# Performance work log

Hardware: AMD Instinct MI355X
Metric: run time of the kernel (lower is better)

The kernel has to match this reference:

```python
import jax, jax.numpy as jnp
import numpy as np

# ---- Clifford algebra Cl(4,1) setup -------------------------------------
SIG = [1, 1, 1, 1, -1]
GA = 1 << len(SIG)  # 32
B, S, E, H = 2, 512, 256, 8
HD = E // H


def _cayley_sign(sig):
    """sign[a,b] such that e_a * e_b = sign[a,b] * e_(a XOR b)."""
    n = len(sig)
    G = 1 << n
    M = np.zeros((G, G), np.float32)
    for a in range(G):
        for b in range(G):
            # canonical reordering sign
            ss = 0
            aa = a >> 1
            while aa:
                ss += bin(aa & b).count('1')
                aa >>= 1
            s = -1.0 if (ss & 1) else 1.0
            # metric contraction on shared basis vectors
            common = a & b
            for i in range(n):
                if (common >> i) & 1:
                    s *= sig[i]
            M[a, b] = s
    return M

SIGN = _cayley_sign(SIG)          # [GA, GA]
SIG_DIAG = np.diag(SIGN).copy()   # blade square signs (metric diagonal)


def _manifold_norm(x):
    # normalize each multivector over its GA components
    return x / jnp.sqrt(jnp.sum(x * x, axis=-1, keepdims=True) + 1e-6)


def _geo_linear(x, w):
    """Clifford linear layer: out[...,o,l] = sum_{i,m,n: m^n=l} w[o,i,m] x[...,i,n] sign(m,n).
    x: [B,S,In,GA], w: [Out,In,GA]. Loop over 32 fixed blades (signed permutation + GEMM)."""
    G = x.shape[-1]
    out = 0.0
    for m in range(G):
        perm = np.arange(G) ^ m              # n = m ^ l
        coeff = jnp.asarray(SIGN[m, perm])   # sign(m, n)
        xs = x[..., perm] * coeff            # [B,S,In,GA]
        out = out + jnp.einsum('oi,bsil->bsol', w[:, :, m], xs)
    return out


def _versor_linear(x, w):
    return _manifold_norm(_geo_linear(x, w))


def _forward(x, mask, wq, wk, wv, wo, gamma):
    b, s = x.shape[0], x.shape[1]
    q = _versor_linear(x, wq).reshape(b, s, H, HD, GA).transpose(0, 2, 1, 3, 4)
    k = _versor_linear(x, wk).reshape(b, s, H, HD, GA).transpose(0, 2, 1, 3, 4)
    v = _versor_linear(x, wv).reshape(b, s, H, HD, GA).transpose(0, 2, 1, 3, 4)
    q_flat = q.reshape(b * H, s, HD, GA)
    k_flat = k.reshape(b * H, s, HD, GA)
    sig_diag = jnp.asarray(SIG_DIAG)
    q_sig = q_flat * sig_diag                      # metric-weighted query
    scalar_score = jnp.einsum('bidl,bjdl->bij', q_sig, k_flat)   # [BH,S,S]
    q_norm_sq = jnp.sum(q_flat ** 2, axis=(-1, -2))[:, :, None]  # [BH,S,1]
    k_norm_sq = jnp.sum(k_flat ** 2, axis=(-1, -2))[:, None, :]  # [BH,1,S]
    bivector_norm = jnp.sqrt(jax.nn.relu(q_norm_sq * k_norm_sq - scalar_score ** 2) + 1e-6)
    score = (scalar_score + gamma * bivector_norm) / np.float32(np.sqrt(HD))
    # triangle update (seq > 1)
    score = score + 0.1 * jnp.matmul(jax.nn.softmax(score, axis=-1), score)
    score = score.reshape(b, H, s, s)
    score = jnp.where(mask[:, None, None, :] == 0, jnp.float32(-1e9), score)
    attn_probs = jax.nn.softmax(score, axis=-1)
    out = jnp.einsum('bhij,bhjdl->bhidl', attn_probs, v)
    out = out.transpose(0, 2, 1, 3, 4).reshape(b, s, E, GA)
    return _versor_linear(out, wo)


def setup_inputs() -> dict:
    key = jax.random.key(0)
    ks = jax.random.split(key, 6)
    std = np.float32((2.0 / (E * GA)) ** 0.5)
    x = jax.random.normal(ks[0], (B, S, E, GA), dtype=jnp.float32)
    wq = jax.random.normal(ks[1], (E, E, GA), dtype=jnp.float32) * std
    wk = jax.random.normal(ks[2], (E, E, GA), dtype=jnp.float32) * std
    wv = jax.random.normal(ks[3], (E, E, GA), dtype=jnp.float32) * std
    wo = jax.random.normal(ks[4], (E, E, GA), dtype=jnp.float32) * std
    gamma = jnp.asarray(0.1, dtype=jnp.float32)
    mask = jnp.ones((B, S), dtype=jnp.int32)
    return {'x': x, 'wq': wq, 'wk': wk, 'wv': wv, 'wo': wo, 'gamma': gamma, 'mask': mask}


def reference(x, wq, wk, wv, wo, gamma, mask):
    return _forward(x, mask, wq, wk, wv, wo, gamma)
```

## Files before the change

kernel.cpp:

```cpp
#include <hip/hip_runtime.h>
#include <stdint.h>

typedef unsigned short u16;
typedef unsigned int u32;
typedef __attribute__((ext_vector_type(8))) __bf16 bf16x8;
typedef __attribute__((ext_vector_type(4))) float f32x4;

#define DEVINL __device__ __forceinline__

DEVINL float bf2f(u16 u){ union{u32 i; float f;} c; c.i = ((u32)u)<<16; return c.f; }
DEVINL u16 f2bf(float f){ union{float f; u32 i;} c; c.f=f; u32 u=c.i; return (u16)((u + 0x7fffu + ((u>>16)&1u))>>16); }
DEVINL u32 pack2(float a, float b){ return (u32)f2bf(a) | ((u32)f2bf(b)<<16); }

DEVINL int sign_neg(int a, int b){
  int s = __popc((a>>1)&b) + __popc((a>>2)&b) + __popc((a>>3)&b) + __popc((a>>4)&b) + ((a&b)>>4);
  return s & 1;
}

struct GTab { int col[32][4]; int ph[32][4]; };
constexpr GTab make_gtab(){
  GTab g{};
  int gc[5][4] = {}; int gp[5][4] = {};
  for (int r=0;r<4;r++){
    const int a=(r>>1)&1, b=r&1;
    gc[0][r]=r^2; gp[0][r]=0;
    gc[1][r]=r^2; gp[1][r]= a?1:3;
    gc[2][r]=r^1; gp[2][r]= a?2:0;
    gc[3][r]=r^1; gp[3][r]=((a?2:0)+(b?1:3))&3;
    gc[4][r]=r;   gp[4][r]=(3+(a?2:0)+(b?2:0))&3;
  }
  for (int I=0;I<32;I++){
    for (int r=0;r<4;r++){ g.col[I][r]=r; g.ph[I][r]=0; }
    for (int bit=0;bit<5;bit++) if ((I>>bit)&1){
      for (int r=0;r<4;r++){
        const int c = g.col[I][r];
        g.ph[I][r]  = (g.ph[I][r] + gp[bit][c]) & 3;
        g.col[I][r] = gc[bit][c];
      }
    }
  }
  return g;
}
constexpr GTab GT = make_gtab();

DEVINL void mv2mat(const float (&x)[32], float (&Mre)[4][4], float (&Mim)[4][4]){
  #pragma unroll
  for (int r=0;r<4;r++)
    #pragma unroll
    for (int c=0;c<4;c++){ Mre[r][c]=0.f; Mim[r][c]=0.f; }
  #pragma unroll
  for (int l=0;l<32;l++){
    #pragma unroll
    for (int r=0;r<4;r++){
      constexpr const GTab& G = GT;
      const int c = G.col[l][r], p = G.ph[l][r];
      if (p==0) Mre[r][c] += x[l];
      else if (p==1) Mim[r][c] += x[l];
      else if (p==2) Mre[r][c] -= x[l];
      else Mim[r][c] -= x[l];
    }
  }
}

DEVINL void mat2mv(const float (&v)[4][8], float (&x)[32]){
  #pragma unroll
  for (int l=0;l<32;l++){
    float s = 0.f;
    #pragma unroll
    for (int r=0;r<4;r++){
      constexpr const GTab& G = GT;
      const int c = G.col[l][r], p = G.ph[l][r];
      if (p==0) s += v[c][r];
      else if (p==1) s += v[c][4+r];
      else if (p==2) s -= v[c][r];
      else s -= v[c][4+r];
    }
    x[l] = 0.25f*s;
  }
}

DEVINL void gload_lds16(const void* g, void* l){
  __builtin_amdgcn_global_load_lds(
    (const __attribute__((address_space(1))) void*)g,
    (__attribute__((address_space(3))) void*)l, 16, 0, 0);
}

__global__ __launch_bounds__(256) void k_v2m(const float* __restrict__ x, u16* __restrict__ Am){
  const int bs = blockIdx.x, i = threadIdx.x;
  const float* xp = x + ((size_t)bs*256 + i)*32;
  float xv[32];
  #pragma unroll
  for (int q=0;q<8;q++){
    float4 v = *(const float4*)(xp + q*4);
    xv[q*4+0]=v.x; xv[q*4+1]=v.y; xv[q*4+2]=v.z; xv[q*4+3]=v.w;
  }
  float Mre[4][4], Mim[4][4];
  mv2mat(xv, Mre, Mim);
  #pragma unroll
  for (int c=0;c<4;c++){
    u32 w0 = pack2(Mre[0][c], Mre[1][c]);
    u32 w1 = pack2(Mre[2][c], Mre[3][c]);
    u32 w2 = pack2(Mim[0][c], Mim[1][c]);
    u32 w3 = pack2(Mim[2][c], Mim[3][c]);
    *(uint4*)(Am + ((size_t)(bs*4+c))*2048 + i*8) = make_uint4(w0,w1,w2,w3);
  }
}

__global__ __launch_bounds__(256) void k_w2m(const float* __restrict__ wq, const float* __restrict__ wk,
                                             const float* __restrict__ wv, const float* __restrict__ wo,
                                             u16* __restrict__ Bfo){
  const int bid = blockIdx.x, i = threadIdx.x;
  const int wsel = bid>>8, o = bid&255;
  const float* w = wsel==0?wq: wsel==1?wk: wsel==2?wv: wo;
  const float* wp = w + ((size_t)o*256 + i)*32;
  float wv32[32];
  #pragma unroll
  for (int q=0;q<8;q++){
    float4 v = *(const float4*)(wp + q*4);
    wv32[q*4+0]=v.x; wv32[q*4+1]=v.y; wv32[q*4+2]=v.z; wv32[q*4+3]=v.w;
  }
  float Wre[4][4], Wim[4][4];
  mv2mat(wv32, Wre, Wim);
  u16* base = Bfo + (size_t)wsel*4194304 + (size_t)(i>>3)*131072 + (o>>1)*1024
            + ((i>>2)&1)*512;
  const int lanebase = (o&1)*8 + (i&3)*16;
  #pragma unroll
  for (int r8=0;r8<8;r8++){
    float e0,e1,e2,e3,e4,e5,e6,e7;
    if (r8<4){
      e0=Wre[r8][0]; e1=Wre[r8][1]; e2=Wre[r8][2]; e3=Wre[r8][3];
      e4=-Wim[r8][0]; e5=-Wim[r8][1]; e6=-Wim[r8][2]; e7=-Wim[r8][3];
    } else {
      e0=Wim[r8-4][0]; e1=Wim[r8-4][1]; e2=Wim[r8-4][2]; e3=Wim[r8-4][3];
      e4=Wre[r8-4][0]; e5=Wre[r8-4][1]; e6=Wre[r8-4][2]; e7=Wre[r8-4][3];
    }
    *(uint4*)(base + (lanebase + r8)*8) =
      make_uint4(pack2(e0,e1), pack2(e2,e3), pack2(e4,e5), pack2(e6,e7));
  }
}

template<int EPI>
__global__ __launch_bounds__(256) void k_mgemm(const u16* __restrict__ Am, const u16* __restrict__ Bfo,
                                               u16* __restrict__ qkv, float* __restrict__ dout,
                                               float* __restrict__ Nqp, float* __restrict__ Nkp){
  constexpr int NT = (EPI==0)?48:16;
  constexpr int NWG = 32*NT;
  __shared__ __align__(16) u16 SM[128*136];
  const int wg = blockIdx.x;
  const int bid = (wg&7)*(NWG/8) + (wg>>3);
  const int tn = bid>>5, tm = bid&31;
  const int row0 = tm*128, col0 = tn*128;
  const int sel   = (EPI==0)? (col0>>11) : 3;
  const int ncol0 = (EPI==0)? (col0&2047) : col0;
  const u16* Wsel = Bfo + (size_t)sel*4194304;
  const int t = threadIdx.x, lane = t&63, wid = t>>6;
  const int wm = wid>>1, wn = wid&1, lo = lane&15, hi = lane>>4;

  int boff[4][2];
  #pragma unroll
  for (int fn=0; fn<4; ++fn){
    const int nblk = (ncol0>>4) + wn*4 + fn;
    #pragma unroll
    for (int kk=0; kk<2; ++kk)
      boff[fn][kk] = (nblk*2+kk)*512 + lane*8;
  }

  f32x4 acc[4][4];
  #pragma unroll
  for(int a=0;a<4;a++){
    #pragma unroll
    for(int b=0;b<4;b++){ acc[a][b] = (f32x4){0.f,0.f,0.f,0.f}; }
  }

  const int sbase = (wid*4)*64;
  #pragma unroll
  for (int cc=0;cc<4;cc++){
    const int base = sbase + cc*64;
    const int idx = base + lane;
    const int rr = idx>>3, g = idx&7;
    gload_lds16(Am + (size_t)(row0+rr)*2048 + ((g^(rr&7))*8), SM + base*8);
  }

  int cbuf = 0;
  for (int kq=0; kq<32; ++kq){
    const u16* Wq = Wsel + (size_t)kq*131072;
    uint4 Br[8];
    #pragma unroll
    for (int fn=0; fn<4; ++fn){
      Br[fn*2+0] = *(const uint4*)(Wq + boff[fn][0]);
      Br[fn*2+1] = *(const uint4*)(Wq + boff[fn][1]);
    }
    if (kq == 0) asm volatile("s_waitcnt vmcnt(8)" ::: "memory");
    else         asm volatile("s_waitcnt vmcnt(4)" ::: "memory");
    __builtin_amdgcn_sched_barrier(0);
    __builtin_amdgcn_s_barrier();
    __builtin_amdgcn_sched_barrier(0);
    if (kq+1 < 32){
      #pragma unroll
      for (int cc=0;cc<4;cc++){
        const int base = sbase + cc*64;
        const int idx = base + lane;
        const int rr = idx>>3, g = idx&7;
        gload_lds16(Am + (size_t)(row0+rr)*2048 + (kq+1)*64 + ((g^(rr&7))*8),
                    SM + (cbuf^1)*8192 + base*8);
      }
    }
    const u16* Ab = SM + cbuf*8192;
    #pragma unroll
    for (int kk=0; kk<2; ++kk){
      bf16x8 af[4];
      #pragma unroll
      for (int f=0;f<4;f++){
        const int ra = wm*64 + f*16 + lo;
        const int jc = kk*4 + hi;
        af[f] = *(const bf16x8*)(Ab + ra*64 + ((jc^(ra&7))*8));
      }
      __builtin_amdgcn_s_setprio(1);
      #pragma unroll
      for (int fm=0;fm<4;fm++){
        #pragma unroll
        for (int fn=0;fn<4;fn++)
          acc[fm][fn] = __builtin_amdgcn_mfma_f32_16x16x32_bf16(
              af[fm], *(const bf16x8*)&Br[fn*2+kk], acc[fm][fn], 0,0,0);
      }
      __builtin_amdgcn_s_setprio(0);
    }
    cbuf ^= 1;
  }

  __syncthreads();
  #pragma unroll
  for (int fm=0;fm<4;fm++){
    #pragma unroll
    for (int r=0;r<4;r++){
      const int mL = wm*64 + fm*16 + hi*4 + r;
      #pragma unroll
      for (int fn=0;fn<4;fn++){
        const int nL = wn*64 + fn*16 + lo;
        SM[mL*136 + nL] = f2bf(acc[fm][fn][r]);
      }
    }
  }
  __syncthreads();
  const int bsL = t>>3, oLp = t&7;
  const int bs = (row0>>2) + bsL;
  const int o0w = ncol0>>3;
  float nsum = 0.f;
  #pragma unroll
  for (int u=0;u<2;u++){
    const int oL = oLp + u*8;
    float v[4][8];
    #pragma unroll
    for (int c=0;c<4;c++){
      uint4 q4 = *(const uint4*)(SM + (bsL*4+c)*136 + oL*8);
      v[c][0]=bf2f((u16)(q4.x&0xffffu)); v[c][1]=bf2f((u16)(q4.x>>16));
      v[c][2]=bf2f((u16)(q4.y&0xffffu)); v[c][3]=bf2f((u16)(q4.y>>16));
      v[c][4]=bf2f((u16)(q4.z&0xffffu)); v[c][5]=bf2f((u16)(q4.z>>16));
      v[c][6]=bf2f((u16)(q4.w&0xffffu)); v[c][7]=bf2f((u16)(q4.w>>16));
    }
    float xs[32];
    mat2mv(v, xs);
    float s = 0.f;
    #pragma unroll
    for (int l=0;l<32;l++) s += xs[l]*xs[l];
    const float rs = rsqrtf(s + 1e-6f);
    if constexpr (EPI==0){
      nsum += s/(s+1e-6f);
      if (sel == 0){
        #pragma unroll
        for (int l=0;l<32;l++) xs[l] = sign_neg(l,l)? -xs[l]*rs : xs[l]*rs;
      } else {
        #pragma unroll
        for (int l=0;l<32;l++) xs[l] *= rs;
      }
      u16* dst = qkv + ((size_t)bs*768 + sel*256 + o0w + oL)*32;
      #pragma unroll
      for (int q=0;q<4;q++)
        *(uint4*)(dst + q*8) = make_uint4(pack2(xs[q*8+0],xs[q*8+1]), pack2(xs[q*8+2],xs[q*8+3]),
                                          pack2(xs[q*8+4],xs[q*8+5]), pack2(xs[q*8+6],xs[q*8+7]));
    } else {
      float* dst = dout + ((size_t)bs*256 + o0w + oL)*32;
      #pragma unroll
      for (int q=0;q<8;q++)
        *(float4*)(dst + q*4) = make_float4(xs[q*4+0]*rs, xs[q*4+1]*rs, xs[q*4+2]*rs, xs[q*4+3]*rs);
    }
  }
  if constexpr (EPI==0){
    if (sel < 2){
      nsum += __shfl_xor(nsum,1); nsum += __shfl_xor(nsum,2); nsum += __shfl_xor(nsum,4);
      if ((t&7)==0){
        const int half = (o0w>>4)&1, h = o0w>>5;
        const int b = bs>>9, s_ = bs&511;
        float* nd = (sel==0)? Nqp : Nkp;
        nd[half*8192 + (b*8+h)*512 + s_] = nsum;
      }
    }
  }
}

DEVINL void mm_steps(const u16* Abase, int Astride, const u16* Bbase, int Bstride, int ksteps,
                     u16* Al, u16* Bl, f32x4 (&acc)[4][4], int lane, int wid){
  const int wm = wid>>1, wn = wid&1, lo = lane&15, hi = lane>>4;
  for (int s=0; s<ksteps; ++s){
    const int k0 = s*64;
    #pragma unroll
    for (int c=0;c<4;c++){
      const int gb = (wid*4+c)*64;
      const int idx = gb + lane;
      const int r = idx>>3, j = idx&7;
      const int sw = ((j^(r&7))*8);
      gload_lds16(Abase + (size_t)r*Astride + k0 + sw, Al + gb*8);
      gload_lds16(Bbase + (size_t)r*Bstride + k0 + sw, Bl + gb*8);
    }
    __syncthreads();
    #pragma unroll
    for (int kk=0; kk<2; ++kk){
      bf16x8 af[4], bfr[4];
      #pragma unroll
      for (int f=0;f<4;f++){
        const int ra = wm*64 + f*16 + lo;
        const int jc = kk*4 + hi;
        af[f] = *(const bf16x8*)(Al + ra*64 + ((jc^(ra&7))*8));
        const int rb = wn*64 + f*16 + lo;
        bfr[f] = *(const bf16x8*)(Bl + rb*64 + ((jc^(rb&7))*8));
      }
      #pragma unroll
      for (int fm=0;fm<4;fm++){
        #pragma unroll
        for (int fn=0;fn<4;fn++)
          acc[fm][fn] = __builtin_amdgcn_mfma_f32_16x16x32_bf16(af[fm], bfr[fn], acc[fm][fn], 0,0,0);
      }
    }
    __syncthreads();
  }
}

__global__ __launch_bounds__(256) void k_score(const u16* __restrict__ qkv, const float* __restrict__ Nqp,
                                               const float* __restrict__ Nkp, const float* __restrict__ gptr,
                                               float* __restrict__ S1, u16* __restrict__ S1T){
  __shared__ __align__(16) u16 Al[128*64];
  __shared__ __align__(16) u16 Bl[128*64];
  __shared__ __align__(16) u16 Tl[128*136];
  const int wg = blockIdx.x;
  const int bid = (wg&7)*32 + (wg>>3);
  const int bh = bid>>4, ti=(bid>>2)&3, tj=bid&3;
  const int b = bh>>3, h = bh&7;
  const int i0=ti*128, j0=tj*128;
  const int t=threadIdx.x, lane=t&63, wid=t>>6;
  const int wm=wid>>1, wn=wid&1, lo=lane&15, hi=lane>>4;
  f32x4 acc[4][4];
  #pragma unroll
  for(int a=0;a<4;a++){
    #pragma unroll
    for(int c=0;c<4;c++){ acc[a][c] = (f32x4){0.f,0.f,0.f,0.f}; }
  }
  const u16* Abase = qkv + ((size_t)(b*512+i0))*24576 + h*1024;
  const u16* Bbase = qkv + ((size_t)(b*512+j0))*24576 + 8192 + h*1024;
  mm_steps(Abase, 24576, Bbase, 24576, 16, Al, Bl, acc, lane, wid);
  const float gamma = *gptr;
  const float rhd = 0.17677669529663687f;
  float nkv[4];
  #pragma unroll
  for (int fn=0;fn<4;fn++){
    const int idx = bh*512 + j0 + wn*64 + fn*16 + lo;
    nkv[fn] = Nkp[idx] + Nkp[8192 + idx];
  }
  #pragma unroll
  for (int fm=0;fm<4;fm++){
    #pragma unroll
    for (int r=0;r<4;r++){
      const int iL = wm*64 + fm*16 + hi*4 + r;
      const int qidx = bh*512 + i0 + iL;
      const float nq = Nqp[qidx] + Nqp[8192 + qidx];
      #pragma unroll
      for (int fn=0;fn<4;fn++){
        const int jL = wn*64 + fn*16 + lo;
        const float ss = acc[fm][fn][r];
        const float biv = sqrtf(fmaxf(nq*nkv[fn] - ss*ss, 0.f) + 1e-6f);
        const float sc = (ss + gamma*biv)*rhd;
        S1[((size_t)bh*512 + i0 + iL)*512 + j0 + jL] = sc;
        Tl[jL*136 + iL] = f2bf(sc);
      }
    }
  }
  __syncthreads();
  const int jj = t>>1, half = t&1;
  u16* dst = S1T + ((size_t)bh*512 + (j0+jj))*512 + i0 + half*64;
  #pragma unroll
  for (int q=0;q<8;q++)
    *(uint4*)(dst + q*8) = *(const uint4*)(Tl + jj*136 + half*64 + q*8);
}

__global__ __launch_bounds__(256) void k_softmax(const float* __restrict__ S, const int* __restrict__ mask,
                                                 u16* __restrict__ P, int masked){
  const int t = threadIdx.x, lane = t&63, wid = t>>6;
  const int row = blockIdx.x*4 + wid;
  const int b = row>>12;
  const float* sp = S + (size_t)row*512;
  float4 a = *(const float4*)(sp + lane*4);
  float4 c = *(const float4*)(sp + 256 + lane*4);
  if (masked){
    const int* mp = mask + b*512;
    int4 ma = *(const int4*)(mp + lane*4);
    int4 mc = *(const int4*)(mp + 256 + lane*4);
    if (ma.x==0) a.x=-1e9f; if (ma.y==0) a.y=-1e9f; if (ma.z==0) a.z=-1e9f; if (ma.w==0) a.w=-1e9f;
    if (mc.x==0) c.x=-1e9f; if (mc.y==0) c.y=-1e9f; if (mc.z==0) c.z=-1e9f; if (mc.w==0) c.w=-1e9f;
  }
  float mx = fmaxf(fmaxf(fmaxf(a.x,a.y),fmaxf(a.z,a.w)), fmaxf(fmaxf(c.x,c.y),fmaxf(c.z,c.w)));
  #pragma unroll
  for (int o=1;o<64;o<<=1) mx = fmaxf(mx, __shfl_xor(mx,o));
  const float e0=__expf(a.x-mx), e1=__expf(a.y-mx), e2=__expf(a.z-mx), e3=__expf(a.w-mx);
  const float e4=__expf(c.x-mx), e5=__expf(c.y-mx), e6=__expf(c.z-mx), e7=__expf(c.w-mx);
  float sm = (e0+e1)+(e2+e3)+(e4+e5)+(e6+e7);
  #pragma unroll
  for (int o=1;o<64;o<<=1) sm += __shfl_xor(sm,o);
  const float inv = 1.f/sm;
  u16* pp = P + (size_t)row*512;
  *(uint2*)(pp + lane*4)       = make_uint2(pack2(e0*inv,e1*inv), pack2(e2*inv,e3*inv));
  *(uint2*)(pp + 256 + lane*4) = make_uint2(pack2(e4*inv,e5*inv), pack2(e6*inv,e7*inv));
}

__global__ __launch_bounds__(256) void k_tri(const u16* __restrict__ P1, const u16* __restrict__ S1T,
                                             float* __restrict__ S1){
  __shared__ __align__(16) u16 Al[128*64];
  __shared__ __align__(16) u16 Bl[128*64];
  const int wg = blockIdx.x;
  const int bid = (wg&7)*32 + (wg>>3);
  const int bh = bid>>4, ti=(bid>>2)&3, tj=bid&3;
  const int i0=ti*128, j0=tj*128;
  const int t=threadIdx.x, lane=t&63, wid=t>>6;
  const int wm=wid>>1, wn=wid&1, lo=lane&15, hi=lane>>4;
  f32x4 acc[4][4];
  #pragma unroll
  for(int a=0;a<4;a++){
    #pragma unroll
    for(int c=0;c<4;c++){ acc[a][c] = (f32x4){0.f,0.f,0.f,0.f}; }
  }
  const u16* Abase = P1  + ((size_t)bh*512 + i0)*512;
  const u16* Bbase = S1T + ((size_t)bh*512 + j0)*512;
  mm_steps(Abase, 512, Bbase, 512, 8, Al, Bl, acc, lane, wid);
  #pragma unroll
  for (int fm=0;fm<4;fm++){
    #pragma unroll
    for (int r=0;r<4;r++){
      const int iL = wm*64 + fm*16 + hi*4 + r;
      #pragma unroll
      for (int fn=0;fn<4;fn++){
        const int jL = wn*64 + fn*16 + lo;
        const size_t idx = ((size_t)bh*512 + i0 + iL)*512 + j0 + jL;
        S1[idx] = S1[idx] + 0.1f*acc[fm][fn][r];
      }
    }
  }
}

__global__ __launch_bounds__(256) void k_tr_v(const u16* __restrict__ qkv, u16* __restrict__ VT){
  __shared__ u16 tile[128*129];
  const int bid=blockIdx.x;
  const int bh = bid>>5, dch=(bid>>2)&7, sch=bid&3;
  const int b=bh>>3, h=bh&7;
  const int d0=dch*128, s0=sch*128;
  const int t=threadIdx.x;
  {
    const int r=t>>1, half=t&1;
    const u16* src = qkv + ((size_t)(b*512+s0+r))*24576 + 16384 + h*1024 + d0 + half*64;
    #pragma unroll
    for (int q=0;q<8;q++){
      uint4 v = *(const uint4*)(src + q*8);
      u16* dp = tile + r*129 + half*64 + q*8;
      dp[0]=(u16)(v.x&0xffffu); dp[1]=(u16)(v.x>>16); dp[2]=(u16)(v.y&0xffffu); dp[3]=(u16)(v.y>>16);
      dp[4]=(u16)(v.z&0xffffu); dp[5]=(u16)(v.z>>16); dp[6]=(u16)(v.w&0xffffu); dp[7]=(u16)(v.w>>16);
    }
  }
  __syncthreads();
  {
    const int rr=t>>1, half=t&1;
    u16* dst = VT + ((size_t)bh*1024 + d0+rr)*512 + s0 + half*64;
    #pragma unroll
    for (int q=0;q<4;q++){
      u32 w[8];
      #pragma unroll
      for (int e=0;e<8;e++){
        const int s = half*64 + q*16 + e*2;
        w[e] = (u32)tile[s*129+rr] | ((u32)tile[(s+1)*129+rr]<<16);
      }
      *(uint4*)(dst + q*16)     = make_uint4(w[0],w[1],w[2],w[3]);
      *(uint4*)(dst + q*16 + 8) = make_uint4(w[4],w[5],w[6],w[7]);
    }
  }
}

__global__ __launch_bounds__(256) void k_pv(const u16* __restrict__ P2, const u16* __restrict__ VT,
                                            u16* __restrict__ Am2){
  __shared__ __align__(16) u16 Al[128*64];
  __shared__ __align__(16) u16 Bl[128*64];
  __shared__ __align__(16) u16 Tl[128*136];
  const int wg = blockIdx.x;
  const int bid = (wg&7)*64 + (wg>>3);
  const int bh = bid>>5, ti=(bid>>3)&3, td=bid&7;
  const int b=bh>>3, h=bh&7;
  const int i0=ti*128, d0=td*128;
  const int t=threadIdx.x, lane=t&63, wid=t>>6;
  const int wm=wid>>1, wn=wid&1, lo=lane&15, hi=lane>>4;
  f32x4 acc[4][4];
  #pragma unroll
  for(int a=0;a<4;a++){
    #pragma unroll
    for(int c=0;c<4;c++){ acc[a][c] = (f32x4){0.f,0.f,0.f,0.f}; }
  }
  const u16* Abase = P2 + ((size_t)bh*512 + i0)*512;
  const u16* Bbase = VT + ((size_t)bh*1024 + d0)*512;
  mm_steps(Abase, 512, Bbase, 512, 8, Al, Bl, acc, lane, wid);
  #pragma unroll
  for (int fm=0;fm<4;fm++){
    #pragma unroll
    for (int r=0;r<4;r++){
      const int sL = wm*64 + fm*16 + hi*4 + r;
      #pragma unroll
      for (int fn=0;fn<4;fn++){
        const int dL = wn*64 + fn*16 + lo;
        Tl[sL*136 + dL] = f2bf(acc[fm][fn][r]);
      }
    }
  }
  __syncthreads();
  #pragma unroll
  for (int u=0;u<2;u++){
    const int idx = t + u*256;
    const int sL = idx>>2, hdL = idx&3;
    const u16* tp = Tl + sL*136 + hdL*32;
    float xv[32];
    #pragma unroll
    for (int q=0;q<4;q++){
      uint4 v = *(const uint4*)(tp + q*8);
      xv[q*8+0]=bf2f((u16)(v.x&0xffffu)); xv[q*8+1]=bf2f((u16)(v.x>>16));
      xv[q*8+2]=bf2f((u16)(v.y&0xffffu)); xv[q*8+3]=bf2f((u16)(v.y>>16));
      xv[q*8+4]=bf2f((u16)(v.z&0xffffu)); xv[q*8+5]=bf2f((u16)(v.z>>16));
      xv[q*8+6]=bf2f((u16)(v.w&0xffffu)); xv[q*8+7]=bf2f((u16)(v.w>>16));
    }
    float Mre[4][4], Mim[4][4];
    mv2mat(xv, Mre, Mim);
    const int e = h*32 + td*4 + hdL;
    const size_t mrow = ((size_t)(b*512 + i0 + sL))*4;
    #pragma unroll
    for (int c=0;c<4;c++){
      u32 w0 = pack2(Mre[0][c], Mre[1][c]);
      u32 w1 = pack2(Mre[2][c], Mre[3][c]);
      u32 w2 = pack2(Mim[0][c], Mim[1][c]);
      u32 w3 = pack2(Mim[2][c], Mim[3][c]);
      *(uint4*)(Am2 + (mrow + c)*2048 + e*8) = make_uint4(w0,w1,w2,w3);
    }
  }
}

extern "C" void kernel_launch(void* const* d_in, const int* in_sizes, int n_in,
                              void* d_out, int out_size, void* d_ws, size_t ws_size,
                              hipStream_t stream) {
  const float* x  = (const float*)d_in[0];
  const float* wq = (const float*)d_in[1];
  const float* wk = (const float*)d_in[2];
  const float* wv = (const float*)d_in[3];
  const float* wo = (const float*)d_in[4];
  const float* gamma = (const float*)d_in[5];
  const int*   mask  = (const int*)d_in[6];
  float* out = (float*)d_out;

  char* ws = (char*)d_ws;
  size_t off = 0;
  auto alloc = [&](size_t n){ char* p = ws + off; off += (n + 255) & ~(size_t)255; return p; };
  u16*  Am  = (u16*) alloc(16777216);
  u16*  Bfo = (u16*) alloc(33554432);
  u16*  qkv = (u16*) alloc(50331648);
  float* Nqp = (float*)alloc(65536);
  float* Nkp = (float*)alloc(65536);
  float* S1 = (float*)alloc(16777216);
  u16*  S1T = (u16*) alloc(8388608);
  u16*  P2  = (u16*) alloc(8388608);
  u16*  P1  = (u16*)Am;
  u16*  VT  = (u16*)S1;
  u16*  Am2 = (u16*)Am;

  k_v2m<<<1024, 256, 0, stream>>>(x, Am);
  k_w2m<<<1024, 256, 0, stream>>>(wq, wk, wv, wo, Bfo);
  k_mgemm<0><<<1536, 256, 0, stream>>>(Am, Bfo, qkv, nullptr, Nqp, Nkp);
  k_score<<<256, 256, 0, stream>>>(qkv, Nqp, Nkp, gamma, S1, S1T);
  k_softmax<<<2048, 256, 0, stream>>>(S1, mask, P1, 0);
  k_tri<<<256, 256, 0, stream>>>(P1, S1T, S1);
  k_softmax<<<2048, 256, 0, stream>>>(S1, mask, P2, 1);
  k_tr_v<<<512, 256, 0, stream>>>(qkv, VT);
  k_pv<<<512, 256, 0, stream>>>(P2, VT, Am2);
  k_mgemm<1><<<512, 256, 0, stream>>>(Am2, Bfo, nullptr, out, nullptr, nullptr);
}
```

Baseline: 301.0 us.

## Software-pipeline B-fragment loads across k-steps and use nontemporal A loads in GEMM

Restructures the GEMM main loop so the first half of each step's B fragments is prefetched one iteration ahead into ping-pong register arrays, while the second half is loaded at the start of the step. The A-tile global-to-LDS loads now use a nontemporal cache policy. The aim is to hide global B-load latency behind MFMA work and to keep the streamed A data from evicting cached weights. The cost is more live registers and a fixed vmcnt wait that relies on the load counts matching.

```diff
diff --git a/kernel.cpp b/kernel.cpp
--- a/kernel.cpp
+++ b/kernel.cpp
@@ -84,6 +84,11 @@
     (const __attribute__((address_space(1))) void*)g,
     (__attribute__((address_space(3))) void*)l, 16, 0, 0);
 }
+DEVINL void gload_lds16_nt(const void* g, void* l){
+  __builtin_amdgcn_global_load_lds(
+    (const __attribute__((address_space(1))) void*)g,
+    (__attribute__((address_space(3))) void*)l, 16, 0, 2);
+}
 
 __global__ __launch_bounds__(256) void k_v2m(const float* __restrict__ x, u16* __restrict__ Am){
   const int bs = blockIdx.x, i = threadIdx.x;
@@ -137,6 +142,66 @@
     *(uint4*)(base + (lanebase + r8)*8) =
       make_uint4(pack2(e0,e1), pack2(e2,e3), pack2(e4,e5), pack2(e6,e7));
   }
+}
+
+DEVINL void mg_phase(int kq, int cbuf, const u16* __restrict__ Wsel, const int (&boff)[4][2],
+                     const u16* __restrict__ Am, int row0, int sbase, int lane,
+                     u16* SM, uint4 (&B0)[4], uint4 (&B0n)[4],
+                     f32x4 (&acc)[4][4], int wm, int wn, int lo, int hi){
+  const u16* Wq = Wsel + (size_t)kq*131072;
+  uint4 B1[4];
+  #pragma unroll
+  for (int fn=0; fn<4; ++fn) B1[fn] = *(const uint4*)(Wq + boff[fn][1]);
+  asm volatile("s_waitcnt vmcnt(8)" ::: "memory");
+  __builtin_amdgcn_sched_barrier(0);
+  __builtin_amdgcn_s_barrier();
+  __builtin_amdgcn_sched_barrier(0);
+  if (kq+1 < 32){
+    #pragma unroll
+    for (int cc=0;cc<4;cc++){
+      const int base = sbase + cc*64;
+      const int idx = base + lane;
+      const int rr = idx>>3, g = idx&7;
+      gload_lds16_nt(Am + (size_t)(row0+rr)*2048 + (kq+1)*64 + ((g^(rr&7))*8),
+                     SM + (cbuf^1)*8192 + base*8);
+    }
+  }
+  const u16* Ab = SM + cbuf*8192;
+  bf16x8 af0[4];
+  #pragma unroll
+  for (int f=0;f<4;f++){
+    const int ra = wm*64 + f*16 + lo;
+    af0[f] = *(const bf16x8*)(Ab + ra*64 + ((hi ^ (ra&7))*8));
+  }
+  if (kq+1 < 32){
+    const u16* Wn = Wq + 131072;
+    #pragma unroll
+    for (int fn=0; fn<4; ++fn) B0n[fn] = *(const uint4*)(Wn + boff[fn][0]);
+  }
+  __builtin_amdgcn_s_setprio(1);
+  #pragma unroll
+  for (int fm=0;fm<4;fm++){
+    #pragma unroll
+    for (int fn=0;fn<4;fn++)
+      acc[fm][fn] = __builtin_amdgcn_mfma_f32_16x16x32_bf16(
+          af0[fm], *(const bf16x8*)&B0[fn], acc[fm][fn], 0,0,0);
+  }
+  __builtin_amdgcn_s_setprio(0);
+  bf16x8 af1[4];
+  #pragma unroll
+  for (int f=0;f<4;f++){
+    const int ra = wm*64 + f*16 + lo;
+    af1[f] = *(const bf16x8*)(Ab + ra*64 + (((4+hi) ^ (ra&7))*8));
+  }
+  __builtin_amdgcn_s_setprio(1);
+  #pragma unroll
+  for (int fm=0;fm<4;fm++){
+    #pragma unroll
+    for (int fn=0;fn<4;fn++)
+      acc[fm][fn] = __builtin_amdgcn_mfma_f32_16x16x32_bf16(
+          af1[fm], *(const bf16x8*)&B1[fn], acc[fm][fn], 0,0,0);
+  }
+  __builtin_amdgcn_s_setprio(0);
 }
 
 template<int EPI>
@@ -178,54 +243,16 @@
     const int base = sbase + cc*64;
     const int idx = base + lane;
     const int rr = idx>>3, g = idx&7;
-    gload_lds16(Am + (size_t)(row0+rr)*2048 + ((g^(rr&7))*8), SM + base*8);
-  }
-
-  int cbuf = 0;
-  for (int kq=0; kq<32; ++kq){
-    const u16* Wq = Wsel + (size_t)kq*131072;
-    uint4 Br[8];
-    #pragma unroll
-    for (int fn=0; fn<4; ++fn){
-      Br[fn*2+0] = *(const uint4*)(Wq + boff[fn][0]);
-      Br[fn*2+1] = *(const uint4*)(Wq + boff[fn][1]);
-    }
-    if (kq == 0) asm volatile("s_waitcnt vmcnt(8)" ::: "memory");
-    else         asm volatile("s_waitcnt vmcnt(4)" ::: "memory");
-    __builtin_amdgcn_sched_barrier(0);
-    __builtin_amdgcn_s_barrier();
-    __builtin_amdgcn_sched_barrier(0);
-    if (kq+1 < 32){
-      #pragma unroll
-      for (int cc=0;cc<4;cc++){
-        const int base = sbase + cc*64;
-        const int idx = base + lane;
-        const int rr = idx>>3, g = idx&7;
-        gload_lds16(Am + (size_t)(row0+rr)*2048 + (kq+1)*64 + ((g^(rr&7))*8),
-                    SM + (cbuf^1)*8192 + base*8);
-      }
-    }
-    const u16* Ab = SM + cbuf*8192;
-    #pragma unroll
-    for (int kk=0; kk<2; ++kk){
-      bf16x8 af[4];
-      #pragma unroll
-      for (int f=0;f<4;f++){
-        const int ra = wm*64 + f*16 + lo;
-        const int jc = kk*4 + hi;
-        af[f] = *(const bf16x8*)(Ab + ra*64 + ((jc^(ra&7))*8));
-      }
-      __builtin_amdgcn_s_setprio(1);
-      #pragma unroll
-      for (int fm=0;fm<4;fm++){
-        #pragma unroll
-        for (int fn=0;fn<4;fn++)
-          acc[fm][fn] = __builtin_amdgcn_mfma_f32_16x16x32_bf16(
-              af[fm], *(const bf16x8*)&Br[fn*2+kk], acc[fm][fn], 0,0,0);
-      }
-      __builtin_amdgcn_s_setprio(0);
-    }
-    cbuf ^= 1;
+    gload_lds16_nt(Am + (size_t)(row0+rr)*2048 + ((g^(rr&7))*8), SM + base*8);
+  }
+  uint4 B0a[4], B0b[4];
+  #pragma unroll
+  for (int fn=0; fn<4; ++fn) B0a[fn] = *(const uint4*)(Wsel + boff[fn][0]);
+
+  #pragma unroll 1
+  for (int kq2=0; kq2<16; ++kq2){
+    mg_phase(2*kq2,   0, Wsel, boff, Am, row0, sbase, lane, SM, B0a, B0b, acc, wm, wn, lo, hi);
+    mg_phase(2*kq2+1, 1, Wsel, boff, Am, row0, sbase, lane, SM, B0b, B0a, acc, wm, wn, lo, hi);
   }
 
   __syncthreads();
```

Result: slower. 365.8 us (+21.5%).
